# Kernel optimization log

Hardware: AMD Instinct MI355X
Metric: run time of the kernel (lower is better)

## Reference

```python
import jax, jax.numpy as jnp
import numpy as np

N = 50000  # num nodes


def _gcn_layer(x, W, b, src, dst, dinv):
    # PyG GCNConv: transform first, then normalized neighbor aggregation
    h = x @ W                                   # [N, out]
    norm = dinv[src] * dinv[dst]                # [E]
    msg = h[src] * norm[:, None]                # gather + scale, [E, out]
    agg = jax.ops.segment_sum(msg, dst, num_segments=N)
    agg = agg + h * (dinv * dinv)[:, None]      # self-loop term (weight 1)
    return agg + b


def setup_inputs() -> dict:
    key = jax.random.key(0)
    ks = jax.random.split(key, 9)
    x = jax.random.normal(ks[0], (N, 256), dtype=jnp.float32)
    edge_index = jax.random.randint(ks[1], (2, 800000), 0, N, dtype=jnp.int64)
    def lin(kw, kb, fan_in, fan_out):
        s = 1.0 / np.sqrt(fan_in)
        W = jax.random.uniform(kw, (fan_in, fan_out), jnp.float32, -s, s)
        b = jax.random.uniform(kb, (fan_out,), jnp.float32, -s, s)
        return W, b
    W0, b0 = lin(ks[2], ks[3], 256, 128)
    W1, b1 = lin(ks[4], ks[5], 128, 128)
    W2, b2 = lin(ks[6], ks[7], 128, 64)
    return {"x": x, "edge_index": edge_index,
            "W0": W0, "b0": b0, "W1": W1, "b1": b1, "W2": W2, "b2": b2}


def reference(x, edge_index, W0, b0, W1, b1, W2, b2):
    src, dst = edge_index[0], edge_index[1]
    # degree with implicit self loops (edge weights = 1)
    deg = jax.ops.segment_sum(jnp.ones_like(dst, dtype=x.dtype), dst,
                              num_segments=N) + 1.0
    dinv = jax.lax.rsqrt(deg)
    h = jax.nn.relu(_gcn_layer(x, W0, b0, src, dst, dinv))
    h = jax.nn.relu(_gcn_layer(h, W1, b1, src, dst, dinv))
    out = _gcn_layer(h, W2, b2, src, dst, dinv)  # no relu on final layer
    return out
```

## Files before the change

kernel.cpp:

```cpp
#include <hip/hip_runtime.h>

#define NNODES 50000
#define NEDGES 800000
#define CHUNK 3125

typedef __attribute__((ext_vector_type(8))) short short8;
typedef __attribute__((ext_vector_type(4))) float floatx4;
typedef __attribute__((ext_vector_type(8))) _Float16 f16x8;

__device__ __forceinline__ void async16(const void* g, void* l) {
    __builtin_amdgcn_global_load_lds(
        (const __attribute__((address_space(1))) unsigned int*)g,
        (__attribute__((address_space(3))) unsigned int*)l, 16, 0, 0);
}

__device__ __forceinline__ void split_bf16(float v, short& hi, short& lo) {
    unsigned u = __float_as_uint(v);
    unsigned hu = u & 0xffff0000u;
    hi = (short)(hu >> 16);
    float r = v - __uint_as_float(hu);
    lo = (short)(__float_as_uint(r) >> 16);
}


#define PREP_WBLK 224
#define PREP_TOT  (PREP_WBLK + 256)

__global__ __launch_bounds__(256) void k_prep(
    const float* __restrict__ W0, short* __restrict__ W0h, short* __restrict__ W0l,
    const float* __restrict__ W1, short* __restrict__ W1h, short* __restrict__ W1l,
    const float* __restrict__ W2, short* __restrict__ W2h, short* __restrict__ W2l,
    const int* __restrict__ dst, int* __restrict__ hist2d) {
    int b = blockIdx.x, t = threadIdx.x;
    if (b < PREP_WBLK) {
        int id = b * 256 + t;
        const float* W; short *Wh, *Wl; int K, F;
        if (id < 32768) { W = W0; Wh = W0h; Wl = W0l; K = 256; F = 128; }
        else if (id < 49152) { id -= 32768; W = W1; Wh = W1h; Wl = W1l; K = 128; F = 128; }
        else if (id < 57344) { id -= 49152; W = W2; Wh = W2h; Wl = W2l; K = 128; F = 64; }
        else return;
        int f = id / K, k = id - f * K;
        short h, l;
        split_bf16(W[(size_t)k * F + f], h, l);
        Wh[id] = h;
        Wl[id] = l;
    } else {
        __shared__ int h[256];
        int bb = b - PREP_WBLK;
        h[t] = 0;
        __syncthreads();
        int e0 = bb * CHUNK;
#pragma unroll
        for (int k = 0; k < 13; k++) {
            int o = k * 256 + t;
            if (o < CHUNK) atomicAdd(&h[dst[e0 + o] >> 8], 1);
        }
        __syncthreads();
        hist2d[bb * 256 + t] = h[t];
    }
}

__global__ __launch_bounds__(256) void k_p2(const int* __restrict__ src,
                                            const int* __restrict__ dst,
                                            const int* __restrict__ hist2d,
                                            unsigned* __restrict__ buck) {
    __shared__ int ex[256], cur[256];
    int t = threadIdx.x, b = blockIdx.x;
    int tot = 0, pre = 0;
    for (int bb = 0; bb < 256; bb++) {
        int v = hist2d[bb * 256 + t];
        tot += v;
        pre += (bb < b) ? v : 0;
    }
    ex[t] = tot;
    __syncthreads();
    for (int o = 1; o < 256; o <<= 1) {
        int xx = (t >= o) ? ex[t - o] : 0;
        __syncthreads();
        ex[t] += xx;
        __syncthreads();
    }
    cur[t] = (ex[t] - tot) + pre;
    __syncthreads();
    int e0 = b * CHUNK;
#pragma unroll
    for (int k = 0; k < 13; k++) {
        int o = k * 256 + t;
        if (o < CHUNK) {
            int s = src[e0 + o], d = dst[e0 + o];
            int p = atomicAdd(&cur[d >> 8], 1);
            buck[p] = (unsigned)s | ((unsigned)(d & 255) << 16);
        }
    }
}

__global__ __launch_bounds__(256) void k_p3(const unsigned* __restrict__ buck,
                                            const int* __restrict__ hist2d,
                                            int* __restrict__ rowptr,
                                            float* __restrict__ dinv,
                                            int* __restrict__ ssrc) {
    __shared__ int ex[256], cur[256], h[256], sS0[1], sS[1];
    int t = threadIdx.x, b = blockIdx.x;
    int tot = 0;
    for (int bb = 0; bb < 256; bb++) tot += hist2d[bb * 256 + t];
    ex[t] = tot;
    __syncthreads();
    for (int o = 1; o < 256; o <<= 1) {
        int xx = (t >= o) ? ex[t - o] : 0;
        __syncthreads();
        ex[t] += xx;
        __syncthreads();
    }
    if (t == b) { sS0[0] = ex[t] - tot; sS[0] = tot; }
    h[t] = 0;
    __syncthreads();
    int s0 = sS0[0], S = sS[0];
    for (int i = t; i < S; i += 256)
        atomicAdd(&h[(buck[s0 + i] >> 16) & 255], 1);
    __syncthreads();
    int v = h[t];
    ex[t] = v;
    __syncthreads();
    for (int o = 1; o < 256; o <<= 1) {
        int xx = (t >= o) ? ex[t - o] : 0;
        __syncthreads();
        ex[t] += xx;
        __syncthreads();
    }
    int excl = ex[t] - v;
    int n = b * 256 + t;
    if (n < NNODES) {
        rowptr[n] = s0 + excl;
        dinv[n] = rsqrtf((float)v + 1.0f);
    }
    if (b == 0 && t == 0) rowptr[NNODES] = NEDGES;
    cur[t] = excl;
    __syncthreads();
    for (int i = t; i < S; i += 256) {
        unsigned pk = buck[s0 + i];
        int dl = (pk >> 16) & 255;
        int p = atomicAdd(&cur[dl], 1);
        ssrc[s0 + p] = (int)(pk & 0xFFFFu);
    }
}


__global__ __launch_bounds__(256) void k_gemm0(
    const float* __restrict__ x, const short* __restrict__ Bh,
    const short* __restrict__ Bl, const float* __restrict__ dinv,
    _Float16* __restrict__ g16) {
    __shared__ __align__(16) short sAh[64 * 64], sAl[64 * 64];
    __shared__ __align__(16) short sBh[128 * 64], sBl[128 * 64];
    const int t = threadIdx.x, lane = t & 63, w = t >> 6;
    const int row0 = blockIdx.x * 64;
    const int lr = lane >> 3, lz = lane & 7;
    const int swz = (lz ^ lr) * 8;
    const int fr = lane & 15, fq = lane >> 4;
    floatx4 acc[8] = {};
    const int ar = t >> 2, ac = t & 3;
    int garow = row0 + ar;
    if (garow >= NNODES) garow = NNODES - 1;
    const float* xrow = x + (size_t)garow * 256 + ac * 16;

    for (int k0 = 0; k0 < 256; k0 += 64) {
        const float4* xp = (const float4*)(xrow + k0);
        float4 f0 = xp[0], f1 = xp[1], f2 = xp[2], f3 = xp[3];
        float va[16] = {f0.x, f0.y, f0.z, f0.w, f1.x, f1.y, f1.z, f1.w,
                        f2.x, f2.y, f2.z, f2.w, f3.x, f3.y, f3.z, f3.w};
        short8 h0, h1, l0, l1;
#pragma unroll
        for (int j = 0; j < 8; j++) {
            short h, l;
            split_bf16(va[j], h, l);     h0[j] = h; l0[j] = l;
            split_bf16(va[8 + j], h, l); h1[j] = h; l1[j] = l;
        }
        int c0 = ac * 2;
        *(short8*)&sAh[ar * 64 + ((c0 ^ (ar & 7)) * 8)] = h0;
        *(short8*)&sAh[ar * 64 + (((c0 + 1) ^ (ar & 7)) * 8)] = h1;
        *(short8*)&sAl[ar * 64 + ((c0 ^ (ar & 7)) * 8)] = l0;
        *(short8*)&sAl[ar * 64 + (((c0 + 1) ^ (ar & 7)) * 8)] = l1;
#pragma unroll
        for (int jj = 0; jj < 4; jj++) {
            int j = w * 4 + jj;
            size_t go = (size_t)(j * 8 + lr) * 256 + k0 + swz;
            async16(&Bh[go], &sBh[j * 512 + lane * 8]);
            async16(&Bl[go], &sBl[j * 512 + lane * 8]);
        }
        __syncthreads();
#pragma unroll
        for (int ks = 0; ks < 2; ks++) {
            int R = w * 16 + fr;
            int ca = ((ks * 4 + fq) ^ (R & 7)) * 8;
            short8 ah = *(const short8*)&sAh[R * 64 + ca];
            short8 al = *(const short8*)&sAl[R * 64 + ca];
#pragma unroll
            for (int nt = 0; nt < 8; nt++) {
                int n = nt * 16 + fr;
                int cb = ((ks * 4 + fq) ^ (n & 7)) * 8;
                short8 bh = *(const short8*)&sBh[n * 64 + cb];
                short8 bl = *(const short8*)&sBl[n * 64 + cb];
                acc[nt] = __builtin_amdgcn_mfma_f32_16x16x32_bf16(ah, bh, acc[nt], 0, 0, 0);
                acc[nt] = __builtin_amdgcn_mfma_f32_16x16x32_bf16(ah, bl, acc[nt], 0, 0, 0);
                acc[nt] = __builtin_amdgcn_mfma_f32_16x16x32_bf16(al, bh, acc[nt], 0, 0, 0);
            }
        }
        __syncthreads();
    }
#pragma unroll
    for (int rr = 0; rr < 4; rr++) {
        int gw = row0 + w * 16 + fq * 4 + rr;
        if (gw < NNODES) {
            float dv = dinv[gw];
#pragma unroll
            for (int nt = 0; nt < 8; nt++)
                g16[(size_t)gw * 128 + nt * 16 + fr] =
                    (_Float16)(acc[nt][rr] * dv);
        }
    }
}


template <int BN>
__global__ __launch_bounds__(256) void k_gemm2(
    const short* __restrict__ Ah, const short* __restrict__ Al,
    const short* __restrict__ Bh, const short* __restrict__ Bl,
    const float* __restrict__ dinv, _Float16* __restrict__ g16, int K) {
    constexpr int BM = 64, BK = 64;
    constexpr int NT = BN / 16;
    __shared__ __align__(16) short sAh[BM * BK], sAl[BM * BK];
    __shared__ __align__(16) short sBh[BN * BK], sBl[BN * BK];

    const int tid = threadIdx.x, lane = tid & 63, w = tid >> 6;
    const int row0 = blockIdx.x * BM;
    const int lr = lane >> 3;
    const int lz = lane & 7;
    const int swz = (lz ^ lr) * 8;
    const int fr = lane & 15, fq = lane >> 4;

    floatx4 acc[NT] = {};

    for (int k0 = 0; k0 < K; k0 += BK) {
#pragma unroll
        for (int jj = 0; jj < 2; jj++) {
            int j = w * 2 + jj;
            int grow = row0 + j * 8 + lr;
            if (grow >= NNODES) grow = NNODES - 1;
            size_t go = (size_t)grow * K + k0 + swz;
            async16(&Ah[go], &sAh[j * 8 * BK + lane * 8]);
            async16(&Al[go], &sAl[j * 8 * BK + lane * 8]);
        }
#pragma unroll
        for (int jj = 0; jj < BN / 32; jj++) {
            int j = w * (BN / 32) + jj;
            size_t go = (size_t)(j * 8 + lr) * K + k0 + swz;
            async16(&Bh[go], &sBh[j * 8 * BK + lane * 8]);
            async16(&Bl[go], &sBl[j * 8 * BK + lane * 8]);
        }
        __syncthreads();

#pragma unroll
        for (int ks = 0; ks < 2; ks++) {
            int R = w * 16 + fr;
            int ca = ((ks * 4 + fq) ^ (R & 7)) * 8;
            short8 ah = *(const short8*)&sAh[R * BK + ca];
            short8 al = *(const short8*)&sAl[R * BK + ca];
#pragma unroll
            for (int nt = 0; nt < NT; nt++) {
                int n = nt * 16 + fr;
                int cb = ((ks * 4 + fq) ^ (n & 7)) * 8;
                short8 bh = *(const short8*)&sBh[n * BK + cb];
                short8 bl = *(const short8*)&sBl[n * BK + cb];
                acc[nt] = __builtin_amdgcn_mfma_f32_16x16x32_bf16(ah, bh, acc[nt], 0, 0, 0);
                acc[nt] = __builtin_amdgcn_mfma_f32_16x16x32_bf16(ah, bl, acc[nt], 0, 0, 0);
                acc[nt] = __builtin_amdgcn_mfma_f32_16x16x32_bf16(al, bh, acc[nt], 0, 0, 0);
            }
        }
        __syncthreads();
    }

#pragma unroll
    for (int rr = 0; rr < 4; rr++) {
        int grow = row0 + w * 16 + fq * 4 + rr;
        if (grow < NNODES) {
            float dv = dinv[grow];
#pragma unroll
            for (int nt = 0; nt < NT; nt++)
                g16[(size_t)grow * BN + nt * 16 + fr] =
                    (_Float16)(acc[nt][rr] * dv);
        }
    }
}


template <int F>
__global__ __launch_bounds__(256) void k_agg(const _Float16* __restrict__ g,
                                             const int* __restrict__ ssrc,
                                             const int* __restrict__ rowptr,
                                             const float* __restrict__ dinv,
                                             const float* __restrict__ bias,
                                             float* __restrict__ outf,
                                             short* __restrict__ oh,
                                             short* __restrict__ ol,
                                             int relu, int writebf) {
    constexpr int F8 = F / 8;
    constexpr int NPB = 256 / F8;
    __shared__ int sED[NPB][64];
    int t = threadIdx.x;
    int ln = t / F8;
    int c8 = t - ln * F8;
    int n = blockIdx.x * NPB + ln;
    bool valid = (n < NNODES);
    int nc = valid ? n : NNODES - 1;

    int e0 = rowptr[nc], e1 = rowptr[nc + 1];
    int deg = e1 - e0;
    int cnt = deg < 64 ? deg : 64;
    for (int i = c8; i < cnt; i += F8) sED[ln][i] = ssrc[e0 + i];
    __syncthreads();

    const f16x8* gp = (const f16x8*)g;
    f16x8 sv = gp[(size_t)nc * F8 + c8];
    float a0[8], a1[8], a2[8], a3[8];
#pragma unroll
    for (int j = 0; j < 8; j++) {
        a0[j] = (float)sv[j];
        a1[j] = 0.f; a2[j] = 0.f; a3[j] = 0.f;
    }
    int i = 0;
    for (; i + 4 <= cnt; i += 4) {
        int s0 = sED[ln][i], s1 = sED[ln][i + 1];
        int s2 = sED[ln][i + 2], s3 = sED[ln][i + 3];
        f16x8 v0 = gp[(size_t)s0 * F8 + c8];
        f16x8 v1 = gp[(size_t)s1 * F8 + c8];
        f16x8 v2 = gp[(size_t)s2 * F8 + c8];
        f16x8 v3 = gp[(size_t)s3 * F8 + c8];
#pragma unroll
        for (int j = 0; j < 8; j++) {
            a0[j] += (float)v0[j];
            a1[j] += (float)v1[j];
            a2[j] += (float)v2[j];
            a3[j] += (float)v3[j];
        }
    }
    for (; i < cnt; i++) {
        int s = sED[ln][i];
        f16x8 v = gp[(size_t)s * F8 + c8];
#pragma unroll
        for (int j = 0; j < 8; j++) a0[j] += (float)v[j];
    }
    for (int e = e0 + 64; e < e1; e++) {
        int s = ssrc[e];
        f16x8 v = gp[(size_t)s * F8 + c8];
#pragma unroll
        for (int j = 0; j < 8; j++) a0[j] += (float)v[j];
    }

    float dv = dinv[nc];
    float o[8];
#pragma unroll
    for (int j = 0; j < 8; j++) {
        float s = (a0[j] + a1[j]) + (a2[j] + a3[j]);
        o[j] = s * dv + bias[c8 * 8 + j];
        if (relu) o[j] = fmaxf(o[j], 0.f);
    }
    if (!valid) return;
    if (writebf) {
        short8 h8, l8;
#pragma unroll
        for (int j = 0; j < 8; j++) {
            short h, l;
            split_bf16(o[j], h, l);
            h8[j] = h; l8[j] = l;
        }
        *(short8*)&oh[(size_t)n * F + c8 * 8] = h8;
        *(short8*)&ol[(size_t)n * F + c8 * 8] = l8;
    } else {
        *(float4*)&outf[(size_t)n * F + c8 * 8] =
            make_float4(o[0], o[1], o[2], o[3]);
        *(float4*)&outf[(size_t)n * F + c8 * 8 + 4] =
            make_float4(o[4], o[5], o[6], o[7]);
    }
}


static inline size_t align256(size_t x) { return (x + 255) & ~(size_t)255; }

extern "C" void kernel_launch(void* const* d_in, const int* in_sizes, int n_in,
                              void* d_out, int out_size, void* d_ws, size_t ws_size,
                              hipStream_t stream) {
    const float* x  = (const float*)d_in[0];
    const int*   ei = (const int*)d_in[1];
    const float* W0 = (const float*)d_in[2];
    const float* b0 = (const float*)d_in[3];
    const float* W1 = (const float*)d_in[4];
    const float* b1 = (const float*)d_in[5];
    const float* W2 = (const float*)d_in[6];
    const float* b2 = (const float*)d_in[7];
    float* out = (float*)d_out;

    const int* src = ei;
    const int* dst = ei + NEDGES;

    char* w = (char*)d_ws;
    size_t off = 0;
    float* dinv    = (float*)(w + off); off = align256(off + NNODES * 4);
    int* rowptr    = (int*)(w + off);   off = align256(off + (NNODES + 1) * 4);
    int* hist2d    = (int*)(w + off);   off = align256(off + 256 * 256 * 4);
    unsigned* buck = (unsigned*)(w + off); off = align256(off + (size_t)NEDGES * 4);
    int* ssrc      = (int*)(w + off);   off = align256(off + (size_t)NEDGES * 4);
    short* W0h     = (short*)(w + off); off = align256(off + 256 * 128 * 2);
    short* W0l     = (short*)(w + off); off = align256(off + 256 * 128 * 2);
    short* W1h     = (short*)(w + off); off = align256(off + 128 * 128 * 2);
    short* W1l     = (short*)(w + off); off = align256(off + 128 * 128 * 2);
    short* W2h     = (short*)(w + off); off = align256(off + 128 * 64 * 2);
    short* W2l     = (short*)(w + off); off = align256(off + 128 * 64 * 2);
    short* ph      = (short*)(w + off); off = align256(off + (size_t)NNODES * 128 * 2);
    short* pl      = (short*)(w + off); off = align256(off + (size_t)NNODES * 128 * 2);
    _Float16* g16  = (_Float16*)(w + off); off = align256(off + (size_t)NNODES * 128 * 2);

    const int MB = (NNODES + 63) / 64;
    const int AB128 = (NNODES + 15) / 16;
    const int AB64  = (NNODES + 31) / 32;

    k_prep<<<PREP_TOT, 256, 0, stream>>>(W0, W0h, W0l, W1, W1h, W1l,
                                         W2, W2h, W2l, dst, hist2d);
    k_p2<<<256, 256, 0, stream>>>(src, dst, hist2d, buck);
    k_p3<<<256, 256, 0, stream>>>(buck, hist2d, rowptr, dinv, ssrc);

    k_gemm0<<<MB, 256, 0, stream>>>(x, W0h, W0l, dinv, g16);
    k_agg<128><<<AB128, 256, 0, stream>>>(g16, ssrc, rowptr, dinv, b0,
                                          (float*)nullptr, ph, pl, 1, 1);
    k_gemm2<128><<<MB, 256, 0, stream>>>(ph, pl, W1h, W1l, dinv, g16, 128);
    k_agg<128><<<AB128, 256, 0, stream>>>(g16, ssrc, rowptr, dinv, b1,
                                          (float*)nullptr, ph, pl, 1, 1);
    k_gemm2<64><<<MB, 256, 0, stream>>>(ph, pl, W2h, W2l, dinv, g16, 128);
    k_agg<64><<<AB64, 256, 0, stream>>>(g16, ssrc, rowptr, dinv, b2,
                                        out, (short*)nullptr, (short*)nullptr, 0, 0);
    (void)in_sizes; (void)n_in; (void)out_size; (void)ws_size;
}
```

Measured before the change: 256.8 us.

## Use one wavefront per node in aggregation and stage bucket scatter in LDS

The aggregation kernel now gives each node a whole 64-lane wavefront. Lanes split across feature chunks and interleaved edge slots, neighbor indices are broadcast via shuffles instead of shared memory, and partial sums are reduced with xor-shuffles. The goal is more memory-level parallelism per node and no block-wide barrier, at the cost of four times as many blocks and cross-lane reduction work. Separately, the bucket-scatter kernel first sorts each chunk locally in LDS and then writes contiguous runs to global memory, so global writes coalesce better instead of landing at scattered atomic positions.

```diff
diff --git a/kernel.cpp b/kernel.cpp
--- a/kernel.cpp
+++ b/kernel.cpp
@@ -64,23 +64,32 @@
                                             const int* __restrict__ dst,
                                             const int* __restrict__ hist2d,
                                             unsigned* __restrict__ buck) {
-    __shared__ int ex[256], cur[256];
+    __shared__ int ex[256], lex[256], lcur[256], delta[256];
+    __shared__ unsigned lbuck[CHUNK];
+    __shared__ int gd[CHUNK];
     int t = threadIdx.x, b = blockIdx.x;
-    int tot = 0, pre = 0;
+    int tot = 0, pre = 0, mine = 0;
     for (int bb = 0; bb < 256; bb++) {
         int v = hist2d[bb * 256 + t];
         tot += v;
         pre += (bb < b) ? v : 0;
+        if (bb == b) mine = v;
     }
     ex[t] = tot;
+    lex[t] = mine;
     __syncthreads();
     for (int o = 1; o < 256; o <<= 1) {
-        int xx = (t >= o) ? ex[t - o] : 0;
-        __syncthreads();
-        ex[t] += xx;
-        __syncthreads();
-    }
-    cur[t] = (ex[t] - tot) + pre;
+        int x1 = (t >= o) ? ex[t - o] : 0;
+        int x2 = (t >= o) ? lex[t - o] : 0;
+        __syncthreads();
+        ex[t] += x1;
+        lex[t] += x2;
+        __syncthreads();
+    }
+    int cur0 = (ex[t] - tot) + pre;
+    int lexcl = lex[t] - mine;
+    lcur[t] = lexcl;
+    delta[t] = cur0 - lexcl;
     __syncthreads();
     int e0 = b * CHUNK;
 #pragma unroll
@@ -88,9 +97,17 @@
         int o = k * 256 + t;
         if (o < CHUNK) {
             int s = src[e0 + o], d = dst[e0 + o];
-            int p = atomicAdd(&cur[d >> 8], 1);
-            buck[p] = (unsigned)s | ((unsigned)(d & 255) << 16);
-        }
+            int bin = d >> 8;
+            int lp = atomicAdd(&lcur[bin], 1);
+            lbuck[lp] = (unsigned)s | ((unsigned)(d & 255) << 16);
+            gd[lp] = delta[bin] + lp;
+        }
+    }
+    __syncthreads();
+#pragma unroll
+    for (int k = 0; k < 13; k++) {
+        int o = k * 256 + t;
+        if (o < CHUNK) buck[gd[o]] = lbuck[o];
     }
 }
 
@@ -303,67 +320,86 @@
                                              short* __restrict__ ol,
                                              int relu, int writebf) {
     constexpr int F8 = F / 8;
-    constexpr int NPB = 256 / F8;
-    __shared__ int sED[NPB][64];
-    int t = threadIdx.x;
-    int ln = t / F8;
-    int c8 = t - ln * F8;
-    int n = blockIdx.x * NPB + ln;
-    bool valid = (n < NNODES);
-    int nc = valid ? n : NNODES - 1;
-
-    int e0 = rowptr[nc], e1 = rowptr[nc + 1];
-    int deg = e1 - e0;
-    int cnt = deg < 64 ? deg : 64;
-    for (int i = c8; i < cnt; i += F8) sED[ln][i] = ssrc[e0 + i];
-    __syncthreads();
+    constexpr int ES = 64 / F8;
+    const int t = threadIdx.x;
+    const int w = t >> 6, lane = t & 63;
+    const int c8 = lane & (F8 - 1);
+    const int es = lane / F8;
+    const int n = blockIdx.x * 4 + w;
+    if (n >= NNODES) return;
+
+    const int e0 = rowptr[n], e1 = rowptr[n + 1];
+    const int deg = e1 - e0;
+    const int cnt = deg < 64 ? deg : 64;
+    int sidx = e0 + (lane < cnt ? lane : 0);
+    if (sidx >= NEDGES) sidx = NEDGES - 1;
+    const int s_held = ssrc[sidx];
 
     const f16x8* gp = (const f16x8*)g;
-    f16x8 sv = gp[(size_t)nc * F8 + c8];
-    float a0[8], a1[8], a2[8], a3[8];
-#pragma unroll
-    for (int j = 0; j < 8; j++) {
-        a0[j] = (float)sv[j];
-        a1[j] = 0.f; a2[j] = 0.f; a3[j] = 0.f;
-    }
-    int i = 0;
-    for (; i + 4 <= cnt; i += 4) {
-        int s0 = sED[ln][i], s1 = sED[ln][i + 1];
-        int s2 = sED[ln][i + 2], s3 = sED[ln][i + 3];
+    float a[8];
+#pragma unroll
+    for (int j = 0; j < 8; j++) a[j] = 0.f;
+    if (es == 0) {
+        f16x8 sv = gp[(size_t)n * F8 + c8];
+#pragma unroll
+        for (int j = 0; j < 8; j++) a[j] = (float)sv[j];
+    }
+
+    const int nfull = cnt / ES;
+    int k = 0;
+    for (; k + 4 <= nfull; k += 4) {
+        int s0 = __shfl(s_held, es + (k + 0) * ES, 64);
+        int s1 = __shfl(s_held, es + (k + 1) * ES, 64);
+        int s2 = __shfl(s_held, es + (k + 2) * ES, 64);
+        int s3 = __shfl(s_held, es + (k + 3) * ES, 64);
         f16x8 v0 = gp[(size_t)s0 * F8 + c8];
         f16x8 v1 = gp[(size_t)s1 * F8 + c8];
         f16x8 v2 = gp[(size_t)s2 * F8 + c8];
         f16x8 v3 = gp[(size_t)s3 * F8 + c8];
 #pragma unroll
-        for (int j = 0; j < 8; j++) {
-            a0[j] += (float)v0[j];
-            a1[j] += (float)v1[j];
-            a2[j] += (float)v2[j];
-            a3[j] += (float)v3[j];
-        }
-    }
-    for (; i < cnt; i++) {
-        int s = sED[ln][i];
+        for (int j = 0; j < 8; j++)
+            a[j] += ((float)v0[j] + (float)v1[j]) +
+                    ((float)v2[j] + (float)v3[j]);
+    }
+    for (; k < nfull; k++) {
+        int s = __shfl(s_held, es + k * ES, 64);
         f16x8 v = gp[(size_t)s * F8 + c8];
 #pragma unroll
-        for (int j = 0; j < 8; j++) a0[j] += (float)v[j];
-    }
-    for (int e = e0 + 64; e < e1; e++) {
+        for (int j = 0; j < 8; j++) a[j] += (float)v[j];
+    }
+    {
+        int i = nfull * ES + es;
+        int s = __shfl(s_held, i < cnt ? i : 0, 64);
+        if (i < cnt) {
+            f16x8 v = gp[(size_t)s * F8 + c8];
+#pragma unroll
+            for (int j = 0; j < 8; j++) a[j] += (float)v[j];
+        }
+    }
+    for (int e = e0 + 64 + es; e < e1; e += ES) {
         int s = ssrc[e];
         f16x8 v = gp[(size_t)s * F8 + c8];
 #pragma unroll
-        for (int j = 0; j < 8; j++) a0[j] += (float)v[j];
-    }
-
-    float dv = dinv[nc];
+        for (int j = 0; j < 8; j++) a[j] += (float)v[j];
+    }
+
+#pragma unroll
+    for (int j = 0; j < 8; j++) {
+        float v = a[j];
+        if (F8 == 8) v += __shfl_xor(v, 8, 64);
+        v += __shfl_xor(v, 16, 64);
+        v += __shfl_xor(v, 32, 64);
+        a[j] = v;
+    }
+    if (es != 0) return;
+
+    float dv = dinv[n];
     float o[8];
 #pragma unroll
     for (int j = 0; j < 8; j++) {
-        float s = (a0[j] + a1[j]) + (a2[j] + a3[j]);
-        o[j] = s * dv + bias[c8 * 8 + j];
+        o[j] = a[j] * dv + bias[c8 * 8 + j];
         if (relu) o[j] = fmaxf(o[j], 0.f);
     }
-    if (!valid) return;
     if (writebf) {
         short8 h8, l8;
 #pragma unroll
@@ -419,8 +455,7 @@
     _Float16* g16  = (_Float16*)(w + off); off = align256(off + (size_t)NNODES * 128 * 2);
 
     const int MB = (NNODES + 63) / 64;
-    const int AB128 = (NNODES + 15) / 16;
-    const int AB64  = (NNODES + 31) / 32;
+    const int AB = (NNODES + 3) / 4;
 
     k_prep<<<PREP_TOT, 256, 0, stream>>>(W0, W0h, W0l, W1, W1h, W1l,
                                          W2, W2h, W2l, dst, hist2d);
@@ -428,13 +463,13 @@
     k_p3<<<256, 256, 0, stream>>>(buck, hist2d, rowptr, dinv, ssrc);
 
     k_gemm0<<<MB, 256, 0, stream>>>(x, W0h, W0l, dinv, g16);
-    k_agg<128><<<AB128, 256, 0, stream>>>(g16, ssrc, rowptr, dinv, b0,
-                                          (float*)nullptr, ph, pl, 1, 1);
+    k_agg<128><<<AB, 256, 0, stream>>>(g16, ssrc, rowptr, dinv, b0,
+                                       (float*)nullptr, ph, pl, 1, 1);
     k_gemm2<128><<<MB, 256, 0, stream>>>(ph, pl, W1h, W1l, dinv, g16, 128);
-    k_agg<128><<<AB128, 256, 0, stream>>>(g16, ssrc, rowptr, dinv, b1,
-                                          (float*)nullptr, ph, pl, 1, 1);
+    k_agg<128><<<AB, 256, 0, stream>>>(g16, ssrc, rowptr, dinv, b1,
+                                       (float*)nullptr, ph, pl, 1, 1);
     k_gemm2<64><<<MB, 256, 0, stream>>>(ph, pl, W2h, W2l, dinv, g16, 128);
-    k_agg<64><<<AB64, 256, 0, stream>>>(g16, ssrc, rowptr, dinv, b2,
-                                        out, (short*)nullptr, (short*)nullptr, 0, 0);
+    k_agg<64><<<AB, 256, 0, stream>>>(g16, ssrc, rowptr, dinv, b2,
+                                      out, (short*)nullptr, (short*)nullptr, 0, 0);
     (void)in_sizes; (void)n_in; (void)out_size; (void)ws_size;
 }
```

Measured after the change: 267.5 us. +4.1%, slower.

## Sort aggregation nodes by degree and stage bucket scatter through LDS

Applied to the files above, without the earlier changes.

Builds a degree histogram in k_p3 and adds a k_scat kernel that produces a permutation of nodes ordered by in-degree. The aggregation kernels then process nodes in that order so that nodes sharing a block have similar edge counts, which reduces wavefront divergence and load imbalance. k_p2 is also changed to sort edges locally in LDS first and then write them to the global buckets in bin-contiguous order, giving more coalesced stores. The cost is an extra kernel launch, an extra indirection per node, and scattered output writes in k_agg, since rows are no longer written in node order.

```diff
diff --git a/kernel.cpp b/kernel.cpp
--- a/kernel.cpp
+++ b/kernel.cpp
@@ -30,7 +30,8 @@
     const float* __restrict__ W0, short* __restrict__ W0h, short* __restrict__ W0l,
     const float* __restrict__ W1, short* __restrict__ W1h, short* __restrict__ W1l,
     const float* __restrict__ W2, short* __restrict__ W2h, short* __restrict__ W2l,
-    const int* __restrict__ dst, int* __restrict__ hist2d) {
+    const int* __restrict__ dst, int* __restrict__ hist2d,
+    int* __restrict__ dhist, int* __restrict__ dcur) {
     int b = blockIdx.x, t = threadIdx.x;
     if (b < PREP_WBLK) {
         int id = b * 256 + t;
@@ -47,6 +48,7 @@
     } else {
         __shared__ int h[256];
         int bb = b - PREP_WBLK;
+        if (bb == 0 && t < 64) { dhist[t] = 0; dcur[t] = 0; }
         h[t] = 0;
         __syncthreads();
         int e0 = bb * CHUNK;
@@ -64,23 +66,32 @@
                                             const int* __restrict__ dst,
                                             const int* __restrict__ hist2d,
                                             unsigned* __restrict__ buck) {
-    __shared__ int ex[256], cur[256];
+    __shared__ int ex[256], lex[256], lcur[256], delta[256];
+    __shared__ unsigned lbuck[CHUNK];
+    __shared__ int gd[CHUNK];
     int t = threadIdx.x, b = blockIdx.x;
-    int tot = 0, pre = 0;
+    int tot = 0, pre = 0, mine = 0;
     for (int bb = 0; bb < 256; bb++) {
         int v = hist2d[bb * 256 + t];
         tot += v;
         pre += (bb < b) ? v : 0;
+        if (bb == b) mine = v;
     }
     ex[t] = tot;
+    lex[t] = mine;
     __syncthreads();
     for (int o = 1; o < 256; o <<= 1) {
-        int xx = (t >= o) ? ex[t - o] : 0;
-        __syncthreads();
-        ex[t] += xx;
-        __syncthreads();
-    }
-    cur[t] = (ex[t] - tot) + pre;
+        int x1 = (t >= o) ? ex[t - o] : 0;
+        int x2 = (t >= o) ? lex[t - o] : 0;
+        __syncthreads();
+        ex[t] += x1;
+        lex[t] += x2;
+        __syncthreads();
+    }
+    int cur0 = (ex[t] - tot) + pre;
+    int lexcl = lex[t] - mine;
+    lcur[t] = lexcl;
+    delta[t] = cur0 - lexcl;
     __syncthreads();
     int e0 = b * CHUNK;
 #pragma unroll
@@ -88,9 +99,17 @@
         int o = k * 256 + t;
         if (o < CHUNK) {
             int s = src[e0 + o], d = dst[e0 + o];
-            int p = atomicAdd(&cur[d >> 8], 1);
-            buck[p] = (unsigned)s | ((unsigned)(d & 255) << 16);
-        }
+            int bin = d >> 8;
+            int lp = atomicAdd(&lcur[bin], 1);
+            lbuck[lp] = (unsigned)s | ((unsigned)(d & 255) << 16);
+            gd[lp] = delta[bin] + lp;
+        }
+    }
+    __syncthreads();
+#pragma unroll
+    for (int k = 0; k < 13; k++) {
+        int o = k * 256 + t;
+        if (o < CHUNK) buck[gd[o]] = lbuck[o];
     }
 }
 
@@ -98,12 +117,14 @@
                                             const int* __restrict__ hist2d,
                                             int* __restrict__ rowptr,
                                             float* __restrict__ dinv,
-                                            int* __restrict__ ssrc) {
-    __shared__ int ex[256], cur[256], h[256], sS0[1], sS[1];
+                                            int* __restrict__ ssrc,
+                                            int* __restrict__ dhist) {
+    __shared__ int ex[256], cur[256], h[256], dh[64], sS0[1], sS[1];
     int t = threadIdx.x, b = blockIdx.x;
     int tot = 0;
     for (int bb = 0; bb < 256; bb++) tot += hist2d[bb * 256 + t];
     ex[t] = tot;
+    if (t < 64) dh[t] = 0;
     __syncthreads();
     for (int o = 1; o < 256; o <<= 1) {
         int xx = (t >= o) ? ex[t - o] : 0;
@@ -132,15 +153,51 @@
     if (n < NNODES) {
         rowptr[n] = s0 + excl;
         dinv[n] = rsqrtf((float)v + 1.0f);
+        atomicAdd(&dh[v < 63 ? v : 63], 1);
     }
     if (b == 0 && t == 0) rowptr[NNODES] = NEDGES;
     cur[t] = excl;
     __syncthreads();
+    if (t < 64 && dh[t]) atomicAdd(&dhist[t], dh[t]);
     for (int i = t; i < S; i += 256) {
         unsigned pk = buck[s0 + i];
         int dl = (pk >> 16) & 255;
         int p = atomicAdd(&cur[dl], 1);
         ssrc[s0 + p] = (int)(pk & 0xFFFFu);
+    }
+}
+
+__global__ __launch_bounds__(256) void k_scat(const int* __restrict__ rowptr,
+                                              const int* __restrict__ dhist,
+                                              int* __restrict__ dcur,
+                                              int* __restrict__ perm) {
+    __shared__ int dbase[64], lhist[64], gb[64];
+    int t = threadIdx.x, b = blockIdx.x;
+    if (t < 64) {
+        dbase[t] = dhist[t];
+        lhist[t] = 0;
+    }
+    __syncthreads();
+    for (int o = 1; o < 64; o <<= 1) {
+        int x = (t >= o && t < 64) ? dbase[t - o] : 0;
+        __syncthreads();
+        if (t < 64) dbase[t] += x;
+        __syncthreads();
+    }
+    int n = b * 256 + t;
+    int bin = 0, lrank = 0;
+    bool valid = (n < NNODES);
+    if (valid) {
+        int deg = rowptr[n + 1] - rowptr[n];
+        bin = deg < 63 ? deg : 63;
+        lrank = atomicAdd(&lhist[bin], 1);
+    }
+    __syncthreads();
+    if (t < 64) gb[t] = lhist[t] ? atomicAdd(&dcur[t], lhist[t]) : 0;
+    __syncthreads();
+    if (valid) {
+        int ebase = dbase[bin] - dhist[bin];
+        perm[ebase + gb[bin] + lrank] = n;
     }
 }
 
@@ -298,6 +355,7 @@
                                              const int* __restrict__ rowptr,
                                              const float* __restrict__ dinv,
                                              const float* __restrict__ bias,
+                                             const int* __restrict__ perm,
                                              float* __restrict__ outf,
                                              short* __restrict__ oh,
                                              short* __restrict__ ol,
@@ -308,9 +366,9 @@
     int t = threadIdx.x;
     int ln = t / F8;
     int c8 = t - ln * F8;
-    int n = blockIdx.x * NPB + ln;
-    bool valid = (n < NNODES);
-    int nc = valid ? n : NNODES - 1;
+    int idx = blockIdx.x * NPB + ln;
+    bool valid = (idx < NNODES);
+    int nc = valid ? perm[idx] : 0;
 
     int e0 = rowptr[nc], e1 = rowptr[nc + 1];
     int deg = e1 - e0;
@@ -372,12 +430,12 @@
             split_bf16(o[j], h, l);
             h8[j] = h; l8[j] = l;
         }
-        *(short8*)&oh[(size_t)n * F + c8 * 8] = h8;
-        *(short8*)&ol[(size_t)n * F + c8 * 8] = l8;
+        *(short8*)&oh[(size_t)nc * F + c8 * 8] = h8;
+        *(short8*)&ol[(size_t)nc * F + c8 * 8] = l8;
     } else {
-        *(float4*)&outf[(size_t)n * F + c8 * 8] =
+        *(float4*)&outf[(size_t)nc * F + c8 * 8] =
             make_float4(o[0], o[1], o[2], o[3]);
-        *(float4*)&outf[(size_t)n * F + c8 * 8 + 4] =
+        *(float4*)&outf[(size_t)nc * F + c8 * 8 + 4] =
             make_float4(o[4], o[5], o[6], o[7]);
     }
 }
@@ -408,6 +466,9 @@
     int* hist2d    = (int*)(w + off);   off = align256(off + 256 * 256 * 4);
     unsigned* buck = (unsigned*)(w + off); off = align256(off + (size_t)NEDGES * 4);
     int* ssrc      = (int*)(w + off);   off = align256(off + (size_t)NEDGES * 4);
+    int* dhist     = (int*)(w + off);   off = align256(off + 64 * 4);
+    int* dcur      = (int*)(w + off);   off = align256(off + 64 * 4);
+    int* perm      = (int*)(w + off);   off = align256(off + NNODES * 4);
     short* W0h     = (short*)(w + off); off = align256(off + 256 * 128 * 2);
     short* W0l     = (short*)(w + off); off = align256(off + 256 * 128 * 2);
     short* W1h     = (short*)(w + off); off = align256(off + 128 * 128 * 2);
@@ -421,20 +482,22 @@
     const int MB = (NNODES + 63) / 64;
     const int AB128 = (NNODES + 15) / 16;
     const int AB64  = (NNODES + 31) / 32;
+    const int SB = (NNODES + 255) / 256;
 
     k_prep<<<PREP_TOT, 256, 0, stream>>>(W0, W0h, W0l, W1, W1h, W1l,
-                                         W2, W2h, W2l, dst, hist2d);
+                                         W2, W2h, W2l, dst, hist2d, dhist, dcur);
     k_p2<<<256, 256, 0, stream>>>(src, dst, hist2d, buck);
-    k_p3<<<256, 256, 0, stream>>>(buck, hist2d, rowptr, dinv, ssrc);
+    k_p3<<<256, 256, 0, stream>>>(buck, hist2d, rowptr, dinv, ssrc, dhist);
+    k_scat<<<SB, 256, 0, stream>>>(rowptr, dhist, dcur, perm);
 
     k_gemm0<<<MB, 256, 0, stream>>>(x, W0h, W0l, dinv, g16);
-    k_agg<128><<<AB128, 256, 0, stream>>>(g16, ssrc, rowptr, dinv, b0,
+    k_agg<128><<<AB128, 256, 0, stream>>>(g16, ssrc, rowptr, dinv, b0, perm,
                                           (float*)nullptr, ph, pl, 1, 1);
     k_gemm2<128><<<MB, 256, 0, stream>>>(ph, pl, W1h, W1l, dinv, g16, 128);
-    k_agg<128><<<AB128, 256, 0, stream>>>(g16, ssrc, rowptr, dinv, b1,
+    k_agg<128><<<AB128, 256, 0, stream>>>(g16, ssrc, rowptr, dinv, b1, perm,
                                           (float*)nullptr, ph, pl, 1, 1);
     k_gemm2<64><<<MB, 256, 0, stream>>>(ph, pl, W2h, W2l, dinv, g16, 128);
-    k_agg<64><<<AB64, 256, 0, stream>>>(g16, ssrc, rowptr, dinv, b2,
+    k_agg<64><<<AB64, 256, 0, stream>>>(g16, ssrc, rowptr, dinv, b2, perm,
                                         out, (short*)nullptr, (short*)nullptr, 0, 0);
     (void)in_sizes; (void)n_in; (void)out_size; (void)ws_size;
 }
```

New measurement: 262.1 us. +2.1%, slower.

## Fuse neighbor aggregation with following layer GEMM into one kernel

Applied to the files above, without the earlier changes.

Replaces the separate aggregation and layer-1/layer-2 GEMM kernels with a fused kernel. Each 32-row block gathers neighbor features, applies bias and ReLU, splits the result to bf16 hi/lo directly in shared memory, then runs the MFMA GEMM against the next weight matrix. This removes the global round trip of the hi/lo bf16 intermediate and two kernel launches. The costs are a smaller 32-row tile with fewer rows per block for the GEMM, and separate ping-pong output buffers.

```diff
diff --git a/kernel.cpp b/kernel.cpp
--- a/kernel.cpp
+++ b/kernel.cpp
@@ -221,55 +221,118 @@
 
 
 template <int BN>
-__global__ __launch_bounds__(256) void k_gemm2(
-    const short* __restrict__ Ah, const short* __restrict__ Al,
+__global__ __launch_bounds__(256) void k_fagg(
+    const _Float16* __restrict__ gin,
+    const int* __restrict__ ssrc,
+    const int* __restrict__ rowptr,
+    const float* __restrict__ dinv,
+    const float* __restrict__ bias,
     const short* __restrict__ Bh, const short* __restrict__ Bl,
-    const float* __restrict__ dinv, _Float16* __restrict__ g16, int K) {
-    constexpr int BM = 64, BK = 64;
-    constexpr int NT = BN / 16;
-    __shared__ __align__(16) short sAh[BM * BK], sAl[BM * BK];
-    __shared__ __align__(16) short sBh[BN * BK], sBl[BN * BK];
-
-    const int tid = threadIdx.x, lane = tid & 63, w = tid >> 6;
+    _Float16* __restrict__ gout) {
+    constexpr int BM = 32;
+    constexpr int NT = BN / 32;
+    __shared__ __align__(16) short sAh[2 * BM * 64], sAl[2 * BM * 64];
+    __shared__ __align__(16) short sBh[BN * 64], sBl[BN * 64];
+    __shared__ int sED[16][64];
+
+    const int t = threadIdx.x, lane = t & 63, w = t >> 6;
     const int row0 = blockIdx.x * BM;
-    const int lr = lane >> 3;
-    const int lz = lane & 7;
+
+    const int ln = t >> 4;
+    const int c8 = t & 15;
+    const f16x8* gp = (const f16x8*)gin;
+#pragma unroll
+    for (int p = 0; p < 2; p++) {
+        int r = p * 16 + ln;
+        int gr = row0 + r;
+        if (gr >= NNODES) gr = NNODES - 1;
+        int e0 = rowptr[gr], e1 = rowptr[gr + 1];
+        int deg = e1 - e0;
+        int cnt = deg < 64 ? deg : 64;
+        for (int i = c8; i < cnt; i += 16) sED[ln][i] = ssrc[e0 + i];
+        __syncthreads();
+
+        f16x8 sv = gp[(size_t)gr * 16 + c8];
+        float a0[8], a1[8], a2[8], a3[8];
+#pragma unroll
+        for (int j = 0; j < 8; j++) {
+            a0[j] = (float)sv[j];
+            a1[j] = 0.f; a2[j] = 0.f; a3[j] = 0.f;
+        }
+        int i = 0;
+        for (; i + 4 <= cnt; i += 4) {
+            int s0 = sED[ln][i], s1 = sED[ln][i + 1];
+            int s2 = sED[ln][i + 2], s3 = sED[ln][i + 3];
+            f16x8 v0 = gp[(size_t)s0 * 16 + c8];
+            f16x8 v1 = gp[(size_t)s1 * 16 + c8];
+            f16x8 v2 = gp[(size_t)s2 * 16 + c8];
+            f16x8 v3 = gp[(size_t)s3 * 16 + c8];
+#pragma unroll
+            for (int j = 0; j < 8; j++) {
+                a0[j] += (float)v0[j];
+                a1[j] += (float)v1[j];
+                a2[j] += (float)v2[j];
+                a3[j] += (float)v3[j];
+            }
+        }
+        for (; i < cnt; i++) {
+            int s = sED[ln][i];
+            f16x8 v = gp[(size_t)s * 16 + c8];
+#pragma unroll
+            for (int j = 0; j < 8; j++) a0[j] += (float)v[j];
+        }
+        for (int e = e0 + 64; e < e1; e++) {
+            int s = ssrc[e];
+            f16x8 v = gp[(size_t)s * 16 + c8];
+#pragma unroll
+            for (int j = 0; j < 8; j++) a0[j] += (float)v[j];
+        }
+
+        float dv = dinv[gr];
+        short8 h8, l8;
+#pragma unroll
+        for (int j = 0; j < 8; j++) {
+            float s = (a0[j] + a1[j]) + (a2[j] + a3[j]);
+            float o = s * dv + bias[c8 * 8 + j];
+            o = fmaxf(o, 0.f);
+            short h, l;
+            split_bf16(o, h, l);
+            h8[j] = h; l8[j] = l;
+        }
+        int kt = c8 >> 3, cg = c8 & 7;
+        int ao = kt * (BM * 64) + r * 64 + ((cg ^ (r & 7)) * 8);
+        *(short8*)&sAh[ao] = h8;
+        *(short8*)&sAl[ao] = l8;
+        __syncthreads();
+    }
+
+    const int fr = lane & 15, fq = lane >> 4;
+    const int lr = lane >> 3, lz = lane & 7;
     const int swz = (lz ^ lr) * 8;
-    const int fr = lane & 15, fq = lane >> 4;
-
+    const int wr = w >> 1, wc = w & 1;
     floatx4 acc[NT] = {};
-
-    for (int k0 = 0; k0 < K; k0 += BK) {
-#pragma unroll
-        for (int jj = 0; jj < 2; jj++) {
-            int j = w * 2 + jj;
-            int grow = row0 + j * 8 + lr;
-            if (grow >= NNODES) grow = NNODES - 1;
-            size_t go = (size_t)grow * K + k0 + swz;
-            async16(&Ah[go], &sAh[j * 8 * BK + lane * 8]);
-            async16(&Al[go], &sAl[j * 8 * BK + lane * 8]);
-        }
+#pragma unroll
+    for (int kt = 0; kt < 2; kt++) {
 #pragma unroll
         for (int jj = 0; jj < BN / 32; jj++) {
             int j = w * (BN / 32) + jj;
-            size_t go = (size_t)(j * 8 + lr) * K + k0 + swz;
-            async16(&Bh[go], &sBh[j * 8 * BK + lane * 8]);
-            async16(&Bl[go], &sBl[j * 8 * BK + lane * 8]);
-        }
-        __syncthreads();
-
+            size_t go = (size_t)(j * 8 + lr) * 128 + kt * 64 + swz;
+            async16(&Bh[go], &sBh[j * 512 + lane * 8]);
+            async16(&Bl[go], &sBl[j * 512 + lane * 8]);
+        }
+        __syncthreads();
 #pragma unroll
         for (int ks = 0; ks < 2; ks++) {
-            int R = w * 16 + fr;
-            int ca = ((ks * 4 + fq) ^ (R & 7)) * 8;
-            short8 ah = *(const short8*)&sAh[R * BK + ca];
-            short8 al = *(const short8*)&sAl[R * BK + ca];
+            int R = wr * 16 + fr;
+            int ca = kt * (BM * 64) + R * 64 + (((ks * 4 + fq) ^ (R & 7)) * 8);
+            short8 ah = *(const short8*)&sAh[ca];
+            short8 al = *(const short8*)&sAl[ca];
 #pragma unroll
             for (int nt = 0; nt < NT; nt++) {
-                int n = nt * 16 + fr;
-                int cb = ((ks * 4 + fq) ^ (n & 7)) * 8;
-                short8 bh = *(const short8*)&sBh[n * BK + cb];
-                short8 bl = *(const short8*)&sBl[n * BK + cb];
+                int n = wc * (BN / 2) + nt * 16 + fr;
+                int cb = n * 64 + (((ks * 4 + fq) ^ (n & 7)) * 8);
+                short8 bh = *(const short8*)&sBh[cb];
+                short8 bl = *(const short8*)&sBl[cb];
                 acc[nt] = __builtin_amdgcn_mfma_f32_16x16x32_bf16(ah, bh, acc[nt], 0, 0, 0);
                 acc[nt] = __builtin_amdgcn_mfma_f32_16x16x32_bf16(ah, bl, acc[nt], 0, 0, 0);
                 acc[nt] = __builtin_amdgcn_mfma_f32_16x16x32_bf16(al, bh, acc[nt], 0, 0, 0);
@@ -280,12 +343,12 @@
 
 #pragma unroll
     for (int rr = 0; rr < 4; rr++) {
-        int grow = row0 + w * 16 + fq * 4 + rr;
+        int grow = row0 + wr * 16 + fq * 4 + rr;
         if (grow < NNODES) {
             float dv = dinv[grow];
 #pragma unroll
             for (int nt = 0; nt < NT; nt++)
-                g16[(size_t)grow * BN + nt * 16 + fr] =
+                gout[(size_t)grow * BN + wc * (BN / 2) + nt * 16 + fr] =
                     (_Float16)(acc[nt][rr] * dv);
         }
     }
@@ -298,10 +361,7 @@
                                              const int* __restrict__ rowptr,
                                              const float* __restrict__ dinv,
                                              const float* __restrict__ bias,
-                                             float* __restrict__ outf,
-                                             short* __restrict__ oh,
-                                             short* __restrict__ ol,
-                                             int relu, int writebf) {
+                                             float* __restrict__ outf) {
     constexpr int F8 = F / 8;
     constexpr int NPB = 256 / F8;
     __shared__ int sED[NPB][64];
@@ -361,25 +421,12 @@
     for (int j = 0; j < 8; j++) {
         float s = (a0[j] + a1[j]) + (a2[j] + a3[j]);
         o[j] = s * dv + bias[c8 * 8 + j];
-        if (relu) o[j] = fmaxf(o[j], 0.f);
     }
     if (!valid) return;
-    if (writebf) {
-        short8 h8, l8;
-#pragma unroll
-        for (int j = 0; j < 8; j++) {
-            short h, l;
-            split_bf16(o[j], h, l);
-            h8[j] = h; l8[j] = l;
-        }
-        *(short8*)&oh[(size_t)n * F + c8 * 8] = h8;
-        *(short8*)&ol[(size_t)n * F + c8 * 8] = l8;
-    } else {
-        *(float4*)&outf[(size_t)n * F + c8 * 8] =
-            make_float4(o[0], o[1], o[2], o[3]);
-        *(float4*)&outf[(size_t)n * F + c8 * 8 + 4] =
-            make_float4(o[4], o[5], o[6], o[7]);
-    }
+    *(float4*)&outf[(size_t)n * F + c8 * 8] =
+        make_float4(o[0], o[1], o[2], o[3]);
+    *(float4*)&outf[(size_t)n * F + c8 * 8 + 4] =
+        make_float4(o[4], o[5], o[6], o[7]);
 }
 
 
@@ -414,27 +461,24 @@
     short* W1l     = (short*)(w + off); off = align256(off + 128 * 128 * 2);
     short* W2h     = (short*)(w + off); off = align256(off + 128 * 64 * 2);
     short* W2l     = (short*)(w + off); off = align256(off + 128 * 64 * 2);
-    short* ph      = (short*)(w + off); off = align256(off + (size_t)NNODES * 128 * 2);
-    short* pl      = (short*)(w + off); off = align256(off + (size_t)NNODES * 128 * 2);
-    _Float16* g16  = (_Float16*)(w + off); off = align256(off + (size_t)NNODES * 128 * 2);
+    _Float16* g16a = (_Float16*)(w + off); off = align256(off + (size_t)NNODES * 128 * 2);
+    _Float16* g16b = (_Float16*)(w + off); off = align256(off + (size_t)NNODES * 128 * 2);
+    _Float16* g16c = (_Float16*)(w + off); off = align256(off + (size_t)NNODES * 64 * 2);
 
     const int MB = (NNODES + 63) / 64;
-    const int AB128 = (NNODES + 15) / 16;
-    const int AB64  = (NNODES + 31) / 32;
+    const int FB = (NNODES + 31) / 32;
+    const int AB64 = (NNODES + 31) / 32;
 
     k_prep<<<PREP_TOT, 256, 0, stream>>>(W0, W0h, W0l, W1, W1h, W1l,
                                          W2, W2h, W2l, dst, hist2d);
     k_p2<<<256, 256, 0, stream>>>(src, dst, hist2d, buck);
     k_p3<<<256, 256, 0, stream>>>(buck, hist2d, rowptr, dinv, ssrc);
 
-    k_gemm0<<<MB, 256, 0, stream>>>(x, W0h, W0l, dinv, g16);
-    k_agg<128><<<AB128, 256, 0, stream>>>(g16, ssrc, rowptr, dinv, b0,
-                                          (float*)nullptr, ph, pl, 1, 1);
-    k_gemm2<128><<<MB, 256, 0, stream>>>(ph, pl, W1h, W1l, dinv, g16, 128);
-    k_agg<128><<<AB128, 256, 0, stream>>>(g16, ssrc, rowptr, dinv, b1,
-                                          (float*)nullptr, ph, pl, 1, 1);
-    k_gemm2<64><<<MB, 256, 0, stream>>>(ph, pl, W2h, W2l, dinv, g16, 128);
-    k_agg<64><<<AB64, 256, 0, stream>>>(g16, ssrc, rowptr, dinv, b2,
-                                        out, (short*)nullptr, (short*)nullptr, 0, 0);
+    k_gemm0<<<MB, 256, 0, stream>>>(x, W0h, W0l, dinv, g16a);
+    k_fagg<128><<<FB, 256, 0, stream>>>(g16a, ssrc, rowptr, dinv, b0,
+                                        W1h, W1l, g16b);
+    k_fagg<64><<<FB, 256, 0, stream>>>(g16b, ssrc, rowptr, dinv, b1,
+                                       W2h, W2l, g16c);
+    k_agg<64><<<AB64, 256, 0, stream>>>(g16c, ssrc, rowptr, dinv, b2, out);
     (void)in_sizes; (void)n_in; (void)out_size; (void)ws_size;
 }
```

After: 252.3 us. About the same (-1.8%).
